# Optimization experiments

Measured on AMD Instinct MI355X. Metric: run time of the kernel, lower is better.

Reference implementation:

```python
import jax, jax.numpy as jnp
import numpy as np

EPS = 1e-5
K = 20

def knn_idx(x, k):
    # x: (B, N, C) -> indices of k nearest neighbors (by negative squared distance, includes self)
    sq = jnp.sum(x * x, axis=-1)                                  # (B, N)
    d = 2.0 * jnp.einsum('bnc,bmc->bnm', x, x) - sq[:, :, None] - sq[:, None, :]
    return jax.lax.top_k(d, k)[1]                                 # (B, N, k)

def edge_conv(x, k, W, g, b, rm, rv):
    # x: (B, N, C); W: (O, 2C); BN params: (O,). Returns (B, N, O).
    idx = knn_idx(x, k)
    feat = jax.vmap(lambda xt, i: xt[i])(x, idx)                  # (B, N, k, C) neighbor gather
    ctr = jnp.broadcast_to(x[:, :, None, :], feat.shape)
    edge = jnp.concatenate([feat - ctr, ctr], axis=-1)            # (B, N, k, 2C)
    h = jnp.einsum('bnkc,oc->bnko', edge, W)                      # 1x1 conv
    h = g * (h - rm) * jax.lax.rsqrt(rv + EPS) + b                # BN (eval, running stats)
    h = jnp.where(h > 0, h, 0.2 * h)                              # LeakyReLU(0.2)
    return jnp.max(h, axis=2)                                     # max over k

def bn(h, g, b, rm, rv):
    return g * (h - rm) * jax.lax.rsqrt(rv + EPS) + b

def lrelu(h):
    return jnp.where(h > 0, h, 0.2 * h)

def _bn_params(key, c):
    k1, k2 = jax.random.split(key)
    g = 1.0 + 0.1 * jax.random.normal(k1, (c,), dtype=jnp.float32)
    b = 0.1 * jax.random.normal(k2, (c,), dtype=jnp.float32)
    return g, b, jnp.zeros((c,), jnp.float32), jnp.ones((c,), jnp.float32)

def setup_inputs() -> dict:
    key = jax.random.key(0)
    ks = jax.random.split(key, 16)
    B, Cin, N = 8, 6, 4096
    d = {'x': jax.random.normal(ks[0], (B, Cin, N), dtype=jnp.float32)}
    def w(k, o, i):
        return jax.random.normal(k, (o, i), dtype=jnp.float32) * (1.0 / np.sqrt(i))
    d['W1'] = w(ks[1], 64, 12);   d['g1'], d['b1'], d['m1'], d['v1'] = _bn_params(ks[2], 64)
    d['W2'] = w(ks[3], 64, 128);  d['g2'], d['b2'], d['m2'], d['v2'] = _bn_params(ks[4], 64)
    d['W3'] = w(ks[5], 128, 128); d['g3'], d['b3'], d['m3'], d['v3'] = _bn_params(ks[6], 128)
    d['W4'] = w(ks[7], 256, 256); d['g4'], d['b4'], d['m4'], d['v4'] = _bn_params(ks[8], 256)
    d['W5'] = w(ks[9], 1024, 512); d['g5'], d['b5'], d['m5'], d['v5'] = _bn_params(ks[10], 1024)
    d['L1'] = w(ks[11], 512, 2048); d['gl1'], d['bl1'], d['ml1'], d['vl1'] = _bn_params(ks[12], 512)
    d['L2'] = w(ks[13], 256, 512); d['L2b'] = jnp.zeros((256,), jnp.float32)
    d['gl2'], d['bl2'], d['ml2'], d['vl2'] = _bn_params(ks[14], 256)
    d['L3'] = w(ks[15], 2, 256);  d['L3b'] = jnp.zeros((2,), jnp.float32)
    return d

def reference(x, W1, g1, b1, m1, v1, W2, g2, b2, m2, v2, W3, g3, b3, m3, v3,
              W4, g4, b4, m4, v4, W5, g5, b5, m5, v5,
              L1, gl1, bl1, ml1, vl1, L2, L2b, gl2, bl2, ml2, vl2, L3, L3b):
    xt = jnp.transpose(x, (0, 2, 1))                              # (B, N, 6)
    x1 = edge_conv(xt, K, W1, g1, b1, m1, v1)                     # (B, N, 64)
    x2 = edge_conv(x1, K, W2, g2, b2, m2, v2)                     # (B, N, 64)
    x3 = edge_conv(x2, K, W3, g3, b3, m3, v3)                     # (B, N, 128)
    x4 = edge_conv(x3, K, W4, g4, b4, m4, v4)                     # (B, N, 256)
    xc = jnp.concatenate([x1, x2, x3, x4], axis=-1)               # (B, N, 512)
    h = lrelu(bn(jnp.einsum('bnc,oc->bno', xc, W5), g5, b5, m5, v5))  # (B, N, 1024)
    pooled = jnp.concatenate([jnp.max(h, axis=1), jnp.mean(h, axis=1)], axis=-1)  # (B, 2048)
    o = lrelu(bn(pooled @ L1.T, gl1, bl1, ml1, vl1))
    o = lrelu(bn(o @ L2.T + L2b, gl2, bl2, ml2, vl2))
    return o @ L3.T + L3b                                         # (B, 2)
```

## Files before the change

### kernel.cpp

```cpp
#include <hip/hip_runtime.h>


#define NPTS   4096
#define NB     8
#define BNR    32768
#define KNN    20
#define EPSBN  1e-5f

__device__ __forceinline__ float lrelu(float x){ return x > 0.f ? x : 0.2f*x; }

__global__ __launch_bounds__(256) void k_transpose_pad(const float* __restrict__ x,
                                                       float* __restrict__ xt){
  int id = blockIdx.x*256 + threadIdx.x;
  int b = id >> 12, n = id & (NPTS-1);
  const float* xb = x + (size_t)b*6*NPTS + n;
  float* o = xt + (size_t)id*8;
#pragma unroll
  for (int c = 0; c < 6; ++c) o[c] = xb[(size_t)c*NPTS];
  o[6] = 0.f; o[7] = 0.f;
}

__global__ __launch_bounds__(256) void k_sqnorm(const float* __restrict__ X, int xstride, int c4,
                                                float* __restrict__ sq){
  int id = blockIdx.x*256 + threadIdx.x;
  const float4* r = (const float4*)(X + (size_t)id*xstride);
  float s = 0.f;
  for (int c = 0; c < c4; ++c){ float4 v = r[c]; s += v.x*v.x + v.y*v.y + v.z*v.z + v.w*v.w; }
  sq[id] = s;
}

__global__ __launch_bounds__(256) void k_dgemm(const float* __restrict__ X, int xstride, int Kdim,
                                               const float* __restrict__ sqv,
                                               float* __restrict__ D){
  const int bi = blockIdx.y, bj = blockIdx.x;
  if (bj < bi) return;
  __shared__ float As[16][132];
  __shared__ float Bs[16][132];
  const int i0 = bi*128, j0 = bj*128;
  const int tid = threadIdx.x, tx = tid & 15, ty = tid >> 4;
  float acc[8][8] = {};
  for (int k0 = 0; k0 < Kdim; k0 += 16){
#pragma unroll
    for (int i = 0; i < 8; ++i){
      int li = tid + 256*i;
      int row = li >> 4, kk = li & 15;
      bool ok = (k0 + kk) < Kdim;
      As[kk][row] = ok ? X[(size_t)(i0+row)*xstride + k0+kk] : 0.f;
      Bs[kk][row] = ok ? X[(size_t)(j0+row)*xstride + k0+kk] : 0.f;
    }
    __syncthreads();
#pragma unroll
    for (int kk = 0; kk < 16; ++kk){
      float a[8], b[8];
      *(float4*)&a[0] = *(const float4*)&As[kk][ty*8];
      *(float4*)&a[4] = *(const float4*)&As[kk][ty*8+4];
      *(float4*)&b[0] = *(const float4*)&Bs[kk][tx*4];
      *(float4*)&b[4] = *(const float4*)&Bs[kk][64 + tx*4];
#pragma unroll
      for (int r = 0; r < 8; ++r)
#pragma unroll
        for (int c = 0; c < 8; ++c)
          acc[r][c] = fmaf(a[r], b[c], acc[r][c]);
    }
    __syncthreads();
  }
  float sj[8];
#pragma unroll
  for (int c = 0; c < 4; ++c){
    sj[c]   = sqv[j0 + tx*4 + c];
    sj[c+4] = sqv[j0 + 64 + tx*4 + c];
  }
  float si[8];
#pragma unroll
  for (int r = 0; r < 8; ++r) si[r] = sqv[i0 + ty*8 + r];
#pragma unroll
  for (int r = 0; r < 8; ++r)
#pragma unroll
    for (int c = 0; c < 8; ++c)
      acc[r][c] = 2.f*acc[r][c] - si[r] - sj[c];
#pragma unroll
  for (int r = 0; r < 8; ++r){
    float* drow = D + (size_t)(i0 + ty*8 + r)*NPTS;
    *(float4*)&drow[j0 + tx*4]      = make_float4(acc[r][0], acc[r][1], acc[r][2], acc[r][3]);
    *(float4*)&drow[j0 + 64 + tx*4] = make_float4(acc[r][4], acc[r][5], acc[r][6], acc[r][7]);
  }
  if (bj > bi){
#pragma unroll
    for (int c = 0; c < 4; ++c){
      float* drow0 = D + (size_t)(j0 + tx*4 + c)*NPTS + i0 + ty*8;
      *(float4*)&drow0[0] = make_float4(acc[0][c], acc[1][c], acc[2][c], acc[3][c]);
      *(float4*)&drow0[4] = make_float4(acc[4][c], acc[5][c], acc[6][c], acc[7][c]);
      float* drow1 = D + (size_t)(j0 + 64 + tx*4 + c)*NPTS + i0 + ty*8;
      *(float4*)&drow1[0] = make_float4(acc[0][c+4], acc[1][c+4], acc[2][c+4], acc[3][c+4]);
      *(float4*)&drow1[4] = make_float4(acc[4][c+4], acc[5][c+4], acc[6][c+4], acc[7][c+4]);
    }
  }
}

__global__ __launch_bounds__(256) void k_scan(const float* __restrict__ D,
                                              int* __restrict__ idx){
  const int lane = threadIdx.x & 63;
  const int wv   = threadIdx.x >> 6;
  const int row  = blockIdx.x*4 + wv;
  const float* drow = D + (size_t)row*NPTS;
  float bv = -1e30f; int bi = -1;
  float thr = -1e30f;
  float dcur = drow[lane];
  for (int m0 = 0; m0 < NPTS; m0 += 64){
    float dnext = (m0 + 64 < NPTS) ? drow[m0 + 64 + lane] : -1e30f;
    unsigned long long mask = __ballot(dcur > thr);
    while (mask){
      int l = __ffsll(mask) - 1;
      mask &= mask - 1;
      float dv = __shfl(dcur, l);
      if (dv > thr){
        float upv = __shfl_up(bv, 1);
        int   upi = __shfl_up(bi, 1);
        if (lane < KNN){
          bool ins  = dv > bv;
          bool insp = (lane > 0) && (dv > upv);
          if (ins){ bv = insp ? upv : dv; bi = insp ? upi : (m0 + l); }
        }
        thr = __shfl(bv, KNN-1);
      }
    }
    dcur = dnext;
  }
  if (lane < KNN) idx[(size_t)row*KNN + lane] = bi;
}

__global__ __launch_bounds__(256) void k_gemm_xw(const float* __restrict__ X, int xstride, int Kdim,
                                                 const float* __restrict__ W, int wstride,
                                                 float* __restrict__ Out, int ostride){
  __shared__ float Xs[16][68];
  __shared__ float Ws[16][68];
  const int m0 = blockIdx.x*64, o0 = blockIdx.y*64;
  const int tid = threadIdx.x, tx = tid & 15, ty = tid >> 4;
  float acc[4][4] = {};
  for (int k0 = 0; k0 < Kdim; k0 += 16){
#pragma unroll
    for (int i = 0; i < 4; ++i){
      int li = tid + 256*i;
      int row = li >> 4, kk = li & 15;
      bool ok = (k0 + kk) < Kdim;
      Xs[kk][row] = ok ? X[(size_t)(m0+row)*xstride + k0+kk] : 0.f;
      Ws[kk][row] = ok ? W[(size_t)(o0+row)*wstride + k0+kk] : 0.f;
    }
    __syncthreads();
#pragma unroll
    for (int kk = 0; kk < 16; ++kk){
      float xa[4], wb[4];
      *(float4*)xa = *(const float4*)&Xs[kk][ty*4];
      *(float4*)wb = *(const float4*)&Ws[kk][tx*4];
#pragma unroll
      for (int i = 0; i < 4; ++i)
#pragma unroll
        for (int j = 0; j < 4; ++j)
          acc[i][j] = fmaf(xa[i], wb[j], acc[i][j]);
    }
    __syncthreads();
  }
#pragma unroll
  for (int i = 0; i < 4; ++i){
    float4 v = make_float4(acc[i][0], acc[i][1], acc[i][2], acc[i][3]);
    *(float4*)&Out[(size_t)(m0+ty*4+i)*ostride + o0 + tx*4] = v;
  }
}

__global__ __launch_bounds__(256) void k_gather_conv(const float* __restrict__ P,
                                                     const float* __restrict__ Q,
                                                     const int* __restrict__ idx,
                                                     const float* __restrict__ g,
                                                     const float* __restrict__ bb,
                                                     const float* __restrict__ rm,
                                                     const float* __restrict__ rv,
                                                     float* __restrict__ Out, int oshift, int choff){
  const int O = 1 << oshift;
  int id = blockIdx.x*256 + threadIdx.x;
  int gn = id >> oshift;
  int o  = id & (O-1);
  int bbase = (gn >> 12) * NPTS;
  const int* ip = idx + (size_t)gn*KNN;
  float vmax = -1e30f, vmin = 1e30f;
#pragma unroll
  for (int k = 0; k < KNN; ++k){
    int m = ip[k];
    float v = P[((size_t)(bbase + m) << oshift) + o];
    vmax = fmaxf(vmax, v);
    vmin = fminf(vmin, v);
  }
  float scale = g[o] * rsqrtf(rv[o] + EPSBN);
  float beta  = bb[o] - rm[o]*scale;
  float R = (scale >= 0.f) ? vmax : vmin;
  float h = R - P[((size_t)gn << oshift) + o] + Q[((size_t)gn << oshift) + o];
  Out[(size_t)gn*512 + choff + o] = lrelu(fmaf(scale, h, beta));
}

__global__ __launch_bounds__(256) void k_gemm_w5_pool(const float* __restrict__ X,
                                                      const float* __restrict__ W,
                                                      const float* __restrict__ g,
                                                      const float* __restrict__ bb,
                                                      const float* __restrict__ rm,
                                                      const float* __restrict__ rv,
                                                      float* __restrict__ pmax,
                                                      float* __restrict__ psum){
  __shared__ float Xs[16][132];
  __shared__ float Ws[16][132];
  __shared__ float red[2][16][128];
  const int m0 = blockIdx.x*128, o0 = blockIdx.y*128;
  const int tid = threadIdx.x, tx = tid & 15, ty = tid >> 4;
  float acc[8][8] = {};
  for (int k0 = 0; k0 < 512; k0 += 16){
#pragma unroll
    for (int i = 0; i < 8; ++i){
      int li = tid + 256*i;
      int row = li >> 4, kk = li & 15;
      Xs[kk][row] = X[(size_t)(m0+row)*512 + k0+kk];
      Ws[kk][row] = W[(size_t)(o0+row)*512 + k0+kk];
    }
    __syncthreads();
#pragma unroll
    for (int kk = 0; kk < 16; ++kk){
      float xa[8], wb[8];
      *(float4*)&xa[0] = *(const float4*)&Xs[kk][ty*8];
      *(float4*)&xa[4] = *(const float4*)&Xs[kk][ty*8+4];
      *(float4*)&wb[0] = *(const float4*)&Ws[kk][tx*4];
      *(float4*)&wb[4] = *(const float4*)&Ws[kk][64 + tx*4];
#pragma unroll
      for (int i = 0; i < 8; ++i)
#pragma unroll
        for (int j = 0; j < 8; ++j)
          acc[i][j] = fmaf(xa[i], wb[j], acc[i][j]);
    }
    __syncthreads();
  }
#pragma unroll
  for (int j = 0; j < 8; ++j){
    int ocol = (j < 4) ? (tx*4 + j) : (64 + tx*4 + j - 4);
    int o = o0 + ocol;
    float scale = g[o] * rsqrtf(rv[o] + EPSBN);
    float beta  = bb[o] - rm[o]*scale;
    float mx = -1e30f, sm = 0.f;
#pragma unroll
    for (int i = 0; i < 8; ++i){
      float h = lrelu(fmaf(scale, acc[i][j], beta));
      mx = fmaxf(mx, h);
      sm += h;
    }
    red[0][ty][ocol] = mx;
    red[1][ty][ocol] = sm;
  }
  __syncthreads();
  if (tid < 128){
    float mx = -1e30f, sm = 0.f;
#pragma unroll
    for (int t = 0; t < 16; ++t){
      mx = fmaxf(mx, red[0][t][tid]);
      sm += red[1][t][tid];
    }
    pmax[(size_t)blockIdx.x*1024 + o0 + tid] = mx;
    psum[(size_t)blockIdx.x*1024 + o0 + tid] = sm;
  }
}

__global__ __launch_bounds__(256) void k_pool_reduce(const float* __restrict__ pmax,
                                                     const float* __restrict__ psum,
                                                     float* __restrict__ pooled){
  int id = blockIdx.x*256 + threadIdx.x;
  int b = id >> 10, o = id & 1023;
  float mx = -1e30f, sm = 0.f;
  for (int t = 0; t < 32; ++t){
    mx = fmaxf(mx, pmax[(size_t)(b*32+t)*1024 + o]);
    sm += psum[(size_t)(b*32+t)*1024 + o];
  }
  pooled[(size_t)b*2048 + o] = mx;
  pooled[(size_t)b*2048 + 1024 + o] = sm * (1.f/NPTS);
}

__global__ __launch_bounds__(256) void k_fc1(const float* __restrict__ pooled,
                                             const float* __restrict__ W,
                                             const float* __restrict__ g,
                                             const float* __restrict__ bb,
                                             const float* __restrict__ rm,
                                             const float* __restrict__ rv,
                                             float* __restrict__ out){
  __shared__ float4 xs[512];
  int b = blockIdx.x >> 1;
  int o = ((blockIdx.x & 1) << 8) + threadIdx.x;
  const float4* pr = (const float4*)(pooled + (size_t)b*2048);
  for (int l = threadIdx.x; l < 512; l += 256) xs[l] = pr[l];
  __syncthreads();
  const float4* wr = (const float4*)(W + (size_t)o*2048);
  float s0=0.f, s1=0.f, s2=0.f, s3=0.f;
#pragma unroll 4
  for (int c = 0; c < 512; ++c){
    float4 w = wr[c], v = xs[c];
    s0 = fmaf(v.x, w.x, s0); s1 = fmaf(v.y, w.y, s1);
    s2 = fmaf(v.z, w.z, s2); s3 = fmaf(v.w, w.w, s3);
  }
  float h = (s0+s1)+(s2+s3);
  float scale = g[o] * rsqrtf(rv[o] + EPSBN);
  float beta  = bb[o] - rm[o]*scale;
  out[(size_t)b*512 + o] = lrelu(fmaf(scale, h, beta));
}

__global__ __launch_bounds__(256) void k_fc2(const float* __restrict__ in,
                                             const float* __restrict__ W,
                                             const float* __restrict__ bias,
                                             const float* __restrict__ g,
                                             const float* __restrict__ bb,
                                             const float* __restrict__ rm,
                                             const float* __restrict__ rv,
                                             float* __restrict__ out){
  __shared__ float4 xs[128];
  int b = blockIdx.x;
  int o = threadIdx.x;
  const float4* pr = (const float4*)(in + (size_t)b*512);
  if (threadIdx.x < 128) xs[threadIdx.x] = pr[threadIdx.x];
  __syncthreads();
  const float4* wr = (const float4*)(W + (size_t)o*512);
  float s0=0.f, s1=0.f, s2=0.f, s3=0.f;
#pragma unroll 4
  for (int c = 0; c < 128; ++c){
    float4 w = wr[c], v = xs[c];
    s0 = fmaf(v.x, w.x, s0); s1 = fmaf(v.y, w.y, s1);
    s2 = fmaf(v.z, w.z, s2); s3 = fmaf(v.w, w.w, s3);
  }
  float h = (s0+s1)+(s2+s3) + bias[o];
  float scale = g[o] * rsqrtf(rv[o] + EPSBN);
  float beta  = bb[o] - rm[o]*scale;
  out[(size_t)b*256 + o] = lrelu(fmaf(scale, h, beta));
}

__global__ __launch_bounds__(64) void k_fc3(const float* __restrict__ in,
                                            const float* __restrict__ W,
                                            const float* __restrict__ bias,
                                            float* __restrict__ out){
  int t = threadIdx.x;
  if (t >= 16) return;
  int b = t >> 1, o = t & 1;
  const float* xr = in + (size_t)b*256;
  const float* wr = W + (size_t)o*256;
  float s = 0.f;
  for (int c = 0; c < 256; ++c) s = fmaf(xr[c], wr[c], s);
  out[b*2 + o] = s + bias[o];
}

extern "C" void kernel_launch(void* const* d_in, const int* in_sizes, int n_in,
                              void* d_out, int out_size, void* d_ws, size_t ws_size,
                              hipStream_t stream){
  (void)in_sizes; (void)n_in; (void)out_size;
  const float* x   = (const float*)d_in[0];
  const float* W1  = (const float*)d_in[1];
  const float* g1  = (const float*)d_in[2];
  const float* b1  = (const float*)d_in[3];
  const float* m1  = (const float*)d_in[4];
  const float* v1  = (const float*)d_in[5];
  const float* W2  = (const float*)d_in[6];
  const float* g2  = (const float*)d_in[7];
  const float* b2  = (const float*)d_in[8];
  const float* m2  = (const float*)d_in[9];
  const float* v2  = (const float*)d_in[10];
  const float* W3  = (const float*)d_in[11];
  const float* g3  = (const float*)d_in[12];
  const float* b3  = (const float*)d_in[13];
  const float* m3  = (const float*)d_in[14];
  const float* v3  = (const float*)d_in[15];
  const float* W4  = (const float*)d_in[16];
  const float* g4  = (const float*)d_in[17];
  const float* b4  = (const float*)d_in[18];
  const float* m4  = (const float*)d_in[19];
  const float* v4  = (const float*)d_in[20];
  const float* W5  = (const float*)d_in[21];
  const float* g5  = (const float*)d_in[22];
  const float* b5  = (const float*)d_in[23];
  const float* m5  = (const float*)d_in[24];
  const float* v5  = (const float*)d_in[25];
  const float* L1  = (const float*)d_in[26];
  const float* gl1 = (const float*)d_in[27];
  const float* bl1 = (const float*)d_in[28];
  const float* ml1 = (const float*)d_in[29];
  const float* vl1 = (const float*)d_in[30];
  const float* L2  = (const float*)d_in[31];
  const float* L2b = (const float*)d_in[32];
  const float* gl2 = (const float*)d_in[33];
  const float* bl2 = (const float*)d_in[34];
  const float* vl2_g = (const float*)d_in[36];
  const float* ml2 = (const float*)d_in[35];
  const float* L3  = (const float*)d_in[37];
  const float* L3b = (const float*)d_in[38];

  float* ws   = (float*)d_ws;
  float* xt   = ws;
  float* sq   = ws + 262144;
  int*   idx  = (int*)(ws + 294912);
  float* Dbuf = ws + 950272;
  float* P    = Dbuf;
  float* Q    = Dbuf + 8388608;
  float* xc   = ws + 17727488;
  float* pmax = ws + 34504704;
  float* psum = ws + 34766848;
  float* pool = ws + 35028992;
  float* oA   = ws + 35045376;
  float* oB   = ws + 35049472;
  if (ws_size < (size_t)35051520 * 4) return;

  k_transpose_pad<<<128, 256, 0, stream>>>(x, xt);

  k_sqnorm<<<128, 256, 0, stream>>>(xt, 8, 2, sq);
  for (int b = 0; b < NB; ++b){
    k_dgemm<<<dim3(32,32), 256, 0, stream>>>(xt + (size_t)b*NPTS*8, 8, 8, sq + b*NPTS, Dbuf);
    k_scan<<<1024, 256, 0, stream>>>(Dbuf, idx + (size_t)b*NPTS*KNN);
  }
  k_gemm_xw<<<dim3(512,1), 256, 0, stream>>>(xt, 8, 6, W1,     12, P, 64);
  k_gemm_xw<<<dim3(512,1), 256, 0, stream>>>(xt, 8, 6, W1 + 6, 12, Q, 64);
  k_gather_conv<<<8192, 256, 0, stream>>>(P, Q, idx, g1, b1, m1, v1, xc, 6, 0);

  k_sqnorm<<<128, 256, 0, stream>>>(xc, 512, 16, sq);
  for (int b = 0; b < NB; ++b){
    k_dgemm<<<dim3(32,32), 256, 0, stream>>>(xc + (size_t)b*NPTS*512, 512, 64, sq + b*NPTS, Dbuf);
    k_scan<<<1024, 256, 0, stream>>>(Dbuf, idx + (size_t)b*NPTS*KNN);
  }
  k_gemm_xw<<<dim3(512,1), 256, 0, stream>>>(xc, 512, 64, W2,      128, P, 64);
  k_gemm_xw<<<dim3(512,1), 256, 0, stream>>>(xc, 512, 64, W2 + 64, 128, Q, 64);
  k_gather_conv<<<8192, 256, 0, stream>>>(P, Q, idx, g2, b2, m2, v2, xc, 6, 64);

  k_sqnorm<<<128, 256, 0, stream>>>(xc + 64, 512, 16, sq);
  for (int b = 0; b < NB; ++b){
    k_dgemm<<<dim3(32,32), 256, 0, stream>>>(xc + 64 + (size_t)b*NPTS*512, 512, 64, sq + b*NPTS, Dbuf);
    k_scan<<<1024, 256, 0, stream>>>(Dbuf, idx + (size_t)b*NPTS*KNN);
  }
  k_gemm_xw<<<dim3(512,2), 256, 0, stream>>>(xc + 64, 512, 64, W3,      128, P, 128);
  k_gemm_xw<<<dim3(512,2), 256, 0, stream>>>(xc + 64, 512, 64, W3 + 64, 128, Q, 128);
  k_gather_conv<<<16384, 256, 0, stream>>>(P, Q, idx, g3, b3, m3, v3, xc, 7, 128);

  k_sqnorm<<<128, 256, 0, stream>>>(xc + 128, 512, 32, sq);
  for (int b = 0; b < NB; ++b){
    k_dgemm<<<dim3(32,32), 256, 0, stream>>>(xc + 128 + (size_t)b*NPTS*512, 512, 128, sq + b*NPTS, Dbuf);
    k_scan<<<1024, 256, 0, stream>>>(Dbuf, idx + (size_t)b*NPTS*KNN);
  }
  k_gemm_xw<<<dim3(512,4), 256, 0, stream>>>(xc + 128, 512, 128, W4,       256, P, 256);
  k_gemm_xw<<<dim3(512,4), 256, 0, stream>>>(xc + 128, 512, 128, W4 + 128, 256, Q, 256);
  k_gather_conv<<<32768, 256, 0, stream>>>(P, Q, idx, g4, b4, m4, v4, xc, 8, 256);

  k_gemm_w5_pool<<<dim3(256,8), 256, 0, stream>>>(xc, W5, g5, b5, m5, v5, pmax, psum);
  k_pool_reduce<<<32, 256, 0, stream>>>(pmax, psum, pool);

  k_fc1<<<16, 256, 0, stream>>>(pool, L1, gl1, bl1, ml1, vl1, oA);
  k_fc2<<<8, 256, 0, stream>>>(oA, L2, L2b, gl2, bl2, ml2, vl2_g, oB);
  k_fc3<<<1, 64, 0, stream>>>(oB, L3, L3b, (float*)d_out);
}
```

Measured before the change: 3.577 ms.

## Drop symmetric dgemm trick, vectorize kNN scan, fuse P/Q projection GEMMs

The distance GEMM now computes every tile directly instead of computing only upper-triangle tiles and writing transposed copies with strided stores. The top-k scan reads float4 per lane, 256 columns per step, and filters each group by the max of its four values. The two per-layer projection GEMMs are merged into one kernel that writes interleaved P|Q rows with larger 128-row tiles, and the gather reads from that combined buffer. Computing every distance tile doubles the GEMM arithmetic in exchange for coalesced stores, and the float4 scan adds per-candidate shuffle overhead.

```diff
diff --git a/kernel.cpp b/kernel.cpp
--- a/kernel.cpp
+++ b/kernel.cpp
@@ -32,11 +32,9 @@
 __global__ __launch_bounds__(256) void k_dgemm(const float* __restrict__ X, int xstride, int Kdim,
                                                const float* __restrict__ sqv,
                                                float* __restrict__ D){
-  const int bi = blockIdx.y, bj = blockIdx.x;
-  if (bj < bi) return;
   __shared__ float As[16][132];
   __shared__ float Bs[16][132];
-  const int i0 = bi*128, j0 = bj*128;
+  const int i0 = blockIdx.y*128, j0 = blockIdx.x*128;
   const int tid = threadIdx.x, tx = tid & 15, ty = tid >> 4;
   float acc[8][8] = {};
   for (int k0 = 0; k0 < Kdim; k0 += 16){
@@ -64,36 +62,23 @@
     }
     __syncthreads();
   }
-  float sj[8];
+  float si[8], sj[8];
+#pragma unroll
+  for (int r = 0; r < 8; ++r) si[r] = sqv[i0 + ty*8 + r];
 #pragma unroll
   for (int c = 0; c < 4; ++c){
     sj[c]   = sqv[j0 + tx*4 + c];
     sj[c+4] = sqv[j0 + 64 + tx*4 + c];
   }
-  float si[8];
-#pragma unroll
-  for (int r = 0; r < 8; ++r) si[r] = sqv[i0 + ty*8 + r];
-#pragma unroll
-  for (int r = 0; r < 8; ++r)
-#pragma unroll
-    for (int c = 0; c < 8; ++c)
-      acc[r][c] = 2.f*acc[r][c] - si[r] - sj[c];
 #pragma unroll
   for (int r = 0; r < 8; ++r){
     float* drow = D + (size_t)(i0 + ty*8 + r)*NPTS;
-    *(float4*)&drow[j0 + tx*4]      = make_float4(acc[r][0], acc[r][1], acc[r][2], acc[r][3]);
-    *(float4*)&drow[j0 + 64 + tx*4] = make_float4(acc[r][4], acc[r][5], acc[r][6], acc[r][7]);
-  }
-  if (bj > bi){
-#pragma unroll
-    for (int c = 0; c < 4; ++c){
-      float* drow0 = D + (size_t)(j0 + tx*4 + c)*NPTS + i0 + ty*8;
-      *(float4*)&drow0[0] = make_float4(acc[0][c], acc[1][c], acc[2][c], acc[3][c]);
-      *(float4*)&drow0[4] = make_float4(acc[4][c], acc[5][c], acc[6][c], acc[7][c]);
-      float* drow1 = D + (size_t)(j0 + 64 + tx*4 + c)*NPTS + i0 + ty*8;
-      *(float4*)&drow1[0] = make_float4(acc[0][c+4], acc[1][c+4], acc[2][c+4], acc[3][c+4]);
-      *(float4*)&drow1[4] = make_float4(acc[4][c+4], acc[5][c+4], acc[6][c+4], acc[7][c+4]);
-    }
+    *(float4*)&drow[j0 + tx*4] =
+      make_float4(2.f*acc[r][0]-si[r]-sj[0], 2.f*acc[r][1]-si[r]-sj[1],
+                  2.f*acc[r][2]-si[r]-sj[2], 2.f*acc[r][3]-si[r]-sj[3]);
+    *(float4*)&drow[j0 + 64 + tx*4] =
+      make_float4(2.f*acc[r][4]-si[r]-sj[4], 2.f*acc[r][5]-si[r]-sj[5],
+                  2.f*acc[r][6]-si[r]-sj[6], 2.f*acc[r][7]-si[r]-sj[7]);
   }
 }
 
@@ -102,58 +87,79 @@
   const int lane = threadIdx.x & 63;
   const int wv   = threadIdx.x >> 6;
   const int row  = blockIdx.x*4 + wv;
-  const float* drow = D + (size_t)row*NPTS;
-  float bv = -1e30f; int bi = -1;
-  float thr = -1e30f;
-  float dcur = drow[lane];
-  for (int m0 = 0; m0 < NPTS; m0 += 64){
-    float dnext = (m0 + 64 < NPTS) ? drow[m0 + 64 + lane] : -1e30f;
-    unsigned long long mask = __ballot(dcur > thr);
+  const float4* drow = (const float4*)(D + (size_t)row*NPTS);
+  float lv = -3e38f; int li = 0;
+  float thr = -3e38f;
+  float4 cur = drow[lane];
+  for (int m0 = 0; m0 < NPTS; m0 += 256){
+    float4 nxt = make_float4(-3e38f,-3e38f,-3e38f,-3e38f);
+    if (m0 + 256 < NPTS) nxt = drow[((m0+256) >> 2) + lane];
+    float mx4 = fmaxf(fmaxf(cur.x, cur.y), fmaxf(cur.z, cur.w));
+    unsigned long long mask = __ballot(mx4 > thr);
     while (mask){
       int l = __ffsll(mask) - 1;
       mask &= mask - 1;
-      float dv = __shfl(dcur, l);
-      if (dv > thr){
-        float upv = __shfl_up(bv, 1);
-        int   upi = __shfl_up(bi, 1);
-        if (lane < KNN){
-          bool ins  = dv > bv;
-          bool insp = (lane > 0) && (dv > upv);
-          if (ins){ bv = insp ? upv : dv; bi = insp ? upi : (m0 + l); }
+      float v0 = __shfl(cur.x, l);
+      float v1 = __shfl(cur.y, l);
+      float v2 = __shfl(cur.z, l);
+      float v3 = __shfl(cur.w, l);
+      int c0 = m0 + 4*l;
+#pragma unroll
+      for (int j = 0; j < 4; ++j){
+        float dv = (j==0) ? v0 : (j==1) ? v1 : (j==2) ? v2 : v3;
+        if (dv > thr){
+          float upv = __shfl_up(lv, 1);
+          int   upi = __shfl_up(li, 1);
+          if (lane < KNN){
+            bool ins  = dv > lv;
+            bool insp = (lane > 0) && (dv > upv);
+            if (ins){ lv = insp ? upv : dv; li = insp ? upi : (c0 + j); }
+          }
+          thr = __shfl(lv, KNN-1);
         }
-        thr = __shfl(bv, KNN-1);
       }
     }
-    dcur = dnext;
-  }
-  if (lane < KNN) idx[(size_t)row*KNN + lane] = bi;
-}
-
-__global__ __launch_bounds__(256) void k_gemm_xw(const float* __restrict__ X, int xstride, int Kdim,
-                                                 const float* __restrict__ W, int wstride,
-                                                 float* __restrict__ Out, int ostride){
-  __shared__ float Xs[16][68];
+    cur = nxt;
+  }
+  if (lane < KNN) idx[(size_t)row*KNN + lane] = li;
+}
+
+__global__ __launch_bounds__(256) void k_gemm_pq(const float* __restrict__ X, int xstride, int Kdim,
+                                                 const float* __restrict__ W, int wstride, int Och,
+                                                 float* __restrict__ PQ){
+  __shared__ float Xs[16][132];
   __shared__ float Ws[16][68];
-  const int m0 = blockIdx.x*64, o0 = blockIdx.y*64;
+  const int m0 = blockIdx.x*128, o0 = blockIdx.y*64;
   const int tid = threadIdx.x, tx = tid & 15, ty = tid >> 4;
-  float acc[4][4] = {};
+  const int O2 = 2*Och;
+  float acc[8][4] = {};
   for (int k0 = 0; k0 < Kdim; k0 += 16){
 #pragma unroll
-    for (int i = 0; i < 4; ++i){
+    for (int i = 0; i < 8; ++i){
       int li = tid + 256*i;
       int row = li >> 4, kk = li & 15;
       bool ok = (k0 + kk) < Kdim;
       Xs[kk][row] = ok ? X[(size_t)(m0+row)*xstride + k0+kk] : 0.f;
-      Ws[kk][row] = ok ? W[(size_t)(o0+row)*wstride + k0+kk] : 0.f;
+    }
+#pragma unroll
+    for (int i = 0; i < 4; ++i){
+      int li = tid + 256*i;
+      int row = li >> 4, kk = li & 15;
+      int orow = o0 + row;
+      const float* wr = (orow < Och) ? (W + (size_t)orow*wstride)
+                                     : (W + (size_t)(orow-Och)*wstride + Kdim);
+      bool ok = (k0 + kk) < Kdim;
+      Ws[kk][row] = ok ? wr[k0+kk] : 0.f;
     }
     __syncthreads();
 #pragma unroll
     for (int kk = 0; kk < 16; ++kk){
-      float xa[4], wb[4];
-      *(float4*)xa = *(const float4*)&Xs[kk][ty*4];
-      *(float4*)wb = *(const float4*)&Ws[kk][tx*4];
-#pragma unroll
-      for (int i = 0; i < 4; ++i)
+      float xa[8], wb[4];
+      *(float4*)&xa[0] = *(const float4*)&Xs[kk][ty*8];
+      *(float4*)&xa[4] = *(const float4*)&Xs[kk][ty*8+4];
+      *(float4*)wb     = *(const float4*)&Ws[kk][tx*4];
+#pragma unroll
+      for (int i = 0; i < 8; ++i)
 #pragma unroll
         for (int j = 0; j < 4; ++j)
           acc[i][j] = fmaf(xa[i], wb[j], acc[i][j]);
@@ -161,14 +167,13 @@
     __syncthreads();
   }
 #pragma unroll
-  for (int i = 0; i < 4; ++i){
+  for (int i = 0; i < 8; ++i){
     float4 v = make_float4(acc[i][0], acc[i][1], acc[i][2], acc[i][3]);
-    *(float4*)&Out[(size_t)(m0+ty*4+i)*ostride + o0 + tx*4] = v;
-  }
-}
-
-__global__ __launch_bounds__(256) void k_gather_conv(const float* __restrict__ P,
-                                                     const float* __restrict__ Q,
+    *(float4*)&PQ[(size_t)(m0+ty*8+i)*O2 + o0 + tx*4] = v;
+  }
+}
+
+__global__ __launch_bounds__(256) void k_gather_conv(const float* __restrict__ PQ,
                                                      const int* __restrict__ idx,
                                                      const float* __restrict__ g,
                                                      const float* __restrict__ bb,
@@ -181,18 +186,19 @@
   int o  = id & (O-1);
   int bbase = (gn >> 12) * NPTS;
   const int* ip = idx + (size_t)gn*KNN;
-  float vmax = -1e30f, vmin = 1e30f;
+  float vmax = -3e38f, vmin = 3e38f;
 #pragma unroll
   for (int k = 0; k < KNN; ++k){
     int m = ip[k];
-    float v = P[((size_t)(bbase + m) << oshift) + o];
+    float v = PQ[((size_t)(bbase + m) << (oshift+1)) + o];
     vmax = fmaxf(vmax, v);
     vmin = fminf(vmin, v);
   }
   float scale = g[o] * rsqrtf(rv[o] + EPSBN);
   float beta  = bb[o] - rm[o]*scale;
   float R = (scale >= 0.f) ? vmax : vmin;
-  float h = R - P[((size_t)gn << oshift) + o] + Q[((size_t)gn << oshift) + o];
+  size_t self = (size_t)gn << (oshift+1);
+  float h = R - PQ[self + o] + PQ[self + O + o];
   Out[(size_t)gn*512 + choff + o] = lrelu(fmaf(scale, h, beta));
 }
 
@@ -240,7 +246,7 @@
     int o = o0 + ocol;
     float scale = g[o] * rsqrtf(rv[o] + EPSBN);
     float beta  = bb[o] - rm[o]*scale;
-    float mx = -1e30f, sm = 0.f;
+    float mx = -3e38f, sm = 0.f;
 #pragma unroll
     for (int i = 0; i < 8; ++i){
       float h = lrelu(fmaf(scale, acc[i][j], beta));
@@ -252,7 +258,7 @@
   }
   __syncthreads();
   if (tid < 128){
-    float mx = -1e30f, sm = 0.f;
+    float mx = -3e38f, sm = 0.f;
 #pragma unroll
     for (int t = 0; t < 16; ++t){
       mx = fmaxf(mx, red[0][t][tid]);
@@ -268,7 +274,7 @@
                                                      float* __restrict__ pooled){
   int id = blockIdx.x*256 + threadIdx.x;
   int b = id >> 10, o = id & 1023;
-  float mx = -1e30f, sm = 0.f;
+  float mx = -3e38f, sm = 0.f;
   for (int t = 0; t < 32; ++t){
     mx = fmaxf(mx, pmax[(size_t)(b*32+t)*1024 + o]);
     sm += psum[(size_t)(b*32+t)*1024 + o];
@@ -385,8 +391,8 @@
   const float* L2b = (const float*)d_in[32];
   const float* gl2 = (const float*)d_in[33];
   const float* bl2 = (const float*)d_in[34];
-  const float* vl2_g = (const float*)d_in[36];
   const float* ml2 = (const float*)d_in[35];
+  const float* vl2 = (const float*)d_in[36];
   const float* L3  = (const float*)d_in[37];
   const float* L3b = (const float*)d_in[38];
 
@@ -395,8 +401,7 @@
   float* sq   = ws + 262144;
   int*   idx  = (int*)(ws + 294912);
   float* Dbuf = ws + 950272;
-  float* P    = Dbuf;
-  float* Q    = Dbuf + 8388608;
+  float* PQ   = Dbuf;
   float* xc   = ws + 17727488;
   float* pmax = ws + 34504704;
   float* psum = ws + 34766848;
@@ -412,41 +417,37 @@
     k_dgemm<<<dim3(32,32), 256, 0, stream>>>(xt + (size_t)b*NPTS*8, 8, 8, sq + b*NPTS, Dbuf);
     k_scan<<<1024, 256, 0, stream>>>(Dbuf, idx + (size_t)b*NPTS*KNN);
   }
-  k_gemm_xw<<<dim3(512,1), 256, 0, stream>>>(xt, 8, 6, W1,     12, P, 64);
-  k_gemm_xw<<<dim3(512,1), 256, 0, stream>>>(xt, 8, 6, W1 + 6, 12, Q, 64);
-  k_gather_conv<<<8192, 256, 0, stream>>>(P, Q, idx, g1, b1, m1, v1, xc, 6, 0);
+  k_gemm_pq<<<dim3(256,2), 256, 0, stream>>>(xt, 8, 6, W1, 12, 64, PQ);
+  k_gather_conv<<<8192, 256, 0, stream>>>(PQ, idx, g1, b1, m1, v1, xc, 6, 0);
 
   k_sqnorm<<<128, 256, 0, stream>>>(xc, 512, 16, sq);
   for (int b = 0; b < NB; ++b){
     k_dgemm<<<dim3(32,32), 256, 0, stream>>>(xc + (size_t)b*NPTS*512, 512, 64, sq + b*NPTS, Dbuf);
     k_scan<<<1024, 256, 0, stream>>>(Dbuf, idx + (size_t)b*NPTS*KNN);
   }
-  k_gemm_xw<<<dim3(512,1), 256, 0, stream>>>(xc, 512, 64, W2,      128, P, 64);
-  k_gemm_xw<<<dim3(512,1), 256, 0, stream>>>(xc, 512, 64, W2 + 64, 128, Q, 64);
-  k_gather_conv<<<8192, 256, 0, stream>>>(P, Q, idx, g2, b2, m2, v2, xc, 6, 64);
+  k_gemm_pq<<<dim3(256,2), 256, 0, stream>>>(xc, 512, 64, W2, 128, 64, PQ);
+  k_gather_conv<<<8192, 256, 0, stream>>>(PQ, idx, g2, b2, m2, v2, xc, 6, 64);
 
   k_sqnorm<<<128, 256, 0, stream>>>(xc + 64, 512, 16, sq);
   for (int b = 0; b < NB; ++b){
     k_dgemm<<<dim3(32,32), 256, 0, stream>>>(xc + 64 + (size_t)b*NPTS*512, 512, 64, sq + b*NPTS, Dbuf);
     k_scan<<<1024, 256, 0, stream>>>(Dbuf, idx + (size_t)b*NPTS*KNN);
   }
-  k_gemm_xw<<<dim3(512,2), 256, 0, stream>>>(xc + 64, 512, 64, W3,      128, P, 128);
-  k_gemm_xw<<<dim3(512,2), 256, 0, stream>>>(xc + 64, 512, 64, W3 + 64, 128, Q, 128);
-  k_gather_conv<<<16384, 256, 0, stream>>>(P, Q, idx, g3, b3, m3, v3, xc, 7, 128);
+  k_gemm_pq<<<dim3(256,4), 256, 0, stream>>>(xc + 64, 512, 64, W3, 128, 128, PQ);
+  k_gather_conv<<<16384, 256, 0, stream>>>(PQ, idx, g3, b3, m3, v3, xc, 7, 128);
 
   k_sqnorm<<<128, 256, 0, stream>>>(xc + 128, 512, 32, sq);
   for (int b = 0; b < NB; ++b){
     k_dgemm<<<dim3(32,32), 256, 0, stream>>>(xc + 128 + (size_t)b*NPTS*512, 512, 128, sq + b*NPTS, Dbuf);
     k_scan<<<1024, 256, 0, stream>>>(Dbuf, idx + (size_t)b*NPTS*KNN);
   }
-  k_gemm_xw<<<dim3(512,4), 256, 0, stream>>>(xc + 128, 512, 128, W4,       256, P, 256);
-  k_gemm_xw<<<dim3(512,4), 256, 0, stream>>>(xc + 128, 512, 128, W4 + 128, 256, Q, 256);
-  k_gather_conv<<<32768, 256, 0, stream>>>(P, Q, idx, g4, b4, m4, v4, xc, 8, 256);
+  k_gemm_pq<<<dim3(256,8), 256, 0, stream>>>(xc + 128, 512, 128, W4, 256, 256, PQ);
+  k_gather_conv<<<32768, 256, 0, stream>>>(PQ, idx, g4, b4, m4, v4, xc, 8, 256);
 
   k_gemm_w5_pool<<<dim3(256,8), 256, 0, stream>>>(xc, W5, g5, b5, m5, v5, pmax, psum);
   k_pool_reduce<<<32, 256, 0, stream>>>(pmax, psum, pool);
 
   k_fc1<<<16, 256, 0, stream>>>(pool, L1, gl1, bl1, ml1, vl1, oA);
-  k_fc2<<<8, 256, 0, stream>>>(oA, L2, L2b, gl2, bl2, ml2, vl2_g, oB);
+  k_fc2<<<8, 256, 0, stream>>>(oA, L2, L2b, gl2, bl2, ml2, vl2, oB);
   k_fc3<<<1, 64, 0, stream>>>(oB, L3, L3b, (float*)d_out);
 }
```

Measured after the change: 3.701 ms. 3.5% more time.
